# Kernel optimization log

Measured on AMD Instinct MI355X. Metric: run time of the kernel, lower is better.

## Reference

```python
import jax, jax.numpy as jnp
import numpy as np

C = 256
NUM_HEADS = 4
HEAD_DIM = C // NUM_HEADS
GROUPS = 32
EPS = 1e-5


def setup_inputs() -> dict:
    key = jax.random.key(0)
    ks = jax.random.split(key, 7)
    B, H, W = 4, 64, 64
    x = jax.random.normal(ks[0], (B, C, H, W), dtype=jnp.float32)
    gn_w = jax.random.normal(ks[1], (C,), dtype=jnp.float32) * 0.02 + 1.0
    gn_b = jax.random.normal(ks[2], (C,), dtype=jnp.float32) * 0.02
    qkv_w = jax.random.normal(ks[3], (3 * C, C), dtype=jnp.float32) * (1.0 / np.sqrt(C))
    qkv_b = jax.random.normal(ks[4], (3 * C,), dtype=jnp.float32) * 0.02
    out_w = jax.random.normal(ks[5], (C, C), dtype=jnp.float32) * (1.0 / np.sqrt(C))
    out_b = jax.random.normal(ks[6], (C,), dtype=jnp.float32) * 0.02
    return {"x": x, "gn_w": gn_w, "gn_b": gn_b, "qkv_w": qkv_w,
            "qkv_b": qkv_b, "out_w": out_w, "out_b": out_b}


def _group_norm(x, w, b):
    # x: [B, C, H, W]; normalize over (C/GROUPS, H, W) per group
    B, Cc, Hh, Ww = x.shape
    xg = x.reshape(B, GROUPS, Cc // GROUPS, Hh, Ww)
    mean = jnp.mean(xg, axis=(2, 3, 4), keepdims=True)
    var = jnp.var(xg, axis=(2, 3, 4), keepdims=True)
    xg = (xg - mean) * jax.lax.rsqrt(var + EPS)
    xn = xg.reshape(B, Cc, Hh, Ww)
    return xn * w[None, :, None, None] + b[None, :, None, None]


def reference(x, gn_w, gn_b, qkv_w, qkv_b, out_w, out_b):
    B, Cc, Hh, Ww = x.shape
    N = Hh * Ww
    h = _group_norm(x, gn_w, gn_b).reshape(B, Cc, N)
    # qkv conv1d (kernel size 1) == pointwise linear over channel dim
    qkv = jnp.einsum('oc,bcn->bon', qkv_w, h) + qkv_b[None, :, None]
    q, k, v = jnp.split(qkv, 3, axis=1)
    q = q.reshape(B, NUM_HEADS, HEAD_DIM, N)
    k = k.reshape(B, NUM_HEADS, HEAD_DIM, N)
    v = v.reshape(B, NUM_HEADS, HEAD_DIM, N)
    scale = 1.0 / np.sqrt(HEAD_DIM)
    attn = jnp.einsum('bhdk,bhdl->bhkl', q, k) * scale  # [B, H, N, N]
    attn = jax.nn.softmax(attn, axis=-1)
    out = jnp.einsum('bhkl,bhdl->bhdk', attn, v)  # [B, H, D, N]
    out = out.reshape(B, Cc, N)
    out = jnp.einsum('oc,bcn->bon', out_w, out) + out_b[None, :, None]
    return x + out.reshape(B, Cc, Hh, Ww)
```

## Files before the change

### kernel.cpp

```cpp
#include <hip/hip_runtime.h>
#include <cstdint>

typedef __bf16 bf16_t;
typedef __bf16 bf16x4 __attribute__((ext_vector_type(4)));
typedef __bf16 bf16x8 __attribute__((ext_vector_type(8)));
typedef float f32x4 __attribute__((ext_vector_type(4)));
typedef unsigned int u32x2 __attribute__((ext_vector_type(2)));
typedef unsigned int u32x4 __attribute__((ext_vector_type(4)));

#define B_ 4
#define C_ 256
#define N_ 4096
#define NH_ 4
#define HD_ 64

static __device__ __forceinline__ f32x4 mfma_bf16(bf16x8 a, bf16x8 b, f32x4 c) {
  return __builtin_amdgcn_mfma_f32_16x16x32_bf16(a, b, c, 0, 0, 0);
}

static __device__ __forceinline__ void async16(const void* g, void* l) {
  __builtin_amdgcn_global_load_lds(
      (__attribute__((address_space(1))) void*)(uintptr_t)g,
      (__attribute__((address_space(3))) void*)(uint32_t)(uintptr_t)l,
      16, 0, 0);
}

static __device__ __forceinline__ float fexp2(float x) {
#if __has_builtin(__builtin_amdgcn_exp2f)
  return __builtin_amdgcn_exp2f(x);
#else
  return exp2f(x);
#endif
}

static __device__ __forceinline__ unsigned pack_bf16(float lo, float hi) {
  bf16x4 t;
  t[0] = (bf16_t)lo;
  t[1] = (bf16_t)hi;
  return *(unsigned*)&t;
}

__global__ __launch_bounds__(256) void k_gn_stats(const float* __restrict__ x,
                                                  const float* __restrict__ gn_w,
                                                  const float* __restrict__ gn_b,
                                                  float* __restrict__ gnscale,
                                                  float* __restrict__ gnshift) {
  const int bg = blockIdx.x;
  const int b = bg >> 5, g = bg & 31;
  const float4* p4 = (const float4*)(x + (size_t)(b * C_ + g * 8) * N_);
  float s = 0.f, ss = 0.f;
  for (int i = threadIdx.x; i < 8192; i += 256) {
    float4 v = p4[i];
    s += (v.x + v.y) + (v.z + v.w);
    ss += (v.x * v.x + v.y * v.y) + (v.z * v.z + v.w * v.w);
  }
  for (int off = 32; off > 0; off >>= 1) {
    s += __shfl_down(s, off);
    ss += __shfl_down(ss, off);
  }
  __shared__ float red_s[4], red_ss[4];
  const int wid = threadIdx.x >> 6, lane = threadIdx.x & 63;
  if (lane == 0) { red_s[wid] = s; red_ss[wid] = ss; }
  __syncthreads();
  if (threadIdx.x < 8) {
    float S = (red_s[0] + red_s[1]) + (red_s[2] + red_s[3]);
    float SS = (red_ss[0] + red_ss[1]) + (red_ss[2] + red_ss[3]);
    float mean = S * (1.f / 32768.f);
    float var = SS * (1.f / 32768.f) - mean * mean;
    float rstd = rsqrtf(var + 1e-5f);
    int c = g * 8 + threadIdx.x;
    float w = gn_w[c];
    gnscale[b * C_ + c] = w * rstd;
    gnshift[b * C_ + c] = gn_b[c] - mean * rstd * w;
  }
}

__global__ __launch_bounds__(256) void k_conv_w(const float* __restrict__ qkv_w,
                                                const float* __restrict__ out_w,
                                                bf16_t* __restrict__ w1,
                                                bf16_t* __restrict__ w2) {
  int i = blockIdx.x * 256 + threadIdx.x;
  if (i < 3 * C_ * C_) w1[i] = (bf16_t)qkv_w[i];
  else w2[i - 3 * C_ * C_] = (bf16_t)out_w[i - 3 * C_ * C_];
}

__global__ __launch_bounds__(256) void k_gn_apply(const float* __restrict__ x,
                                                  const float* __restrict__ gnscale,
                                                  const float* __restrict__ gnshift,
                                                  bf16_t* __restrict__ h) {
  __shared__ bf16_t T[32 * 258];
  const int t = threadIdx.x;
  const int tok0 = blockIdx.x * 32;
  const int b = tok0 >> 12;
  const int n0 = tok0 & (N_ - 1);
  const int nl = t & 31, cset = t >> 5;
  const float* xb = x + ((size_t)(b * C_ + cset * 32) << 12) + n0 + nl;
  const float* scp = gnscale + b * C_ + cset * 32;
  const float* shp = gnshift + b * C_ + cset * 32;
#pragma unroll
  for (int j = 0; j < 32; ++j) {
    float y = xb[(size_t)j << 12] * scp[j] + shp[j];
    T[nl * 258 + cset * 32 + j] = (bf16_t)y;
  }
  __syncthreads();
  const int c4 = t & 63;
#pragma unroll
  for (int p = 0; p < 8; ++p) {
    const int tokl = p * 4 + (t >> 6);
    const int idx = tokl * 258 + c4 * 4;
    uint2 v;
    v.x = *(const unsigned*)&T[idx];
    v.y = *(const unsigned*)&T[idx + 2];
    *(uint2*)(h + ((size_t)(tok0 + tokl) << 8) + c4 * 4) = v;
  }
}

__global__ __launch_bounds__(256) void k_gemm_qkv(const bf16_t* __restrict__ h,
                                                  const bf16_t* __restrict__ w1,
                                                  const float* __restrict__ qkv_b,
                                                  bf16_t* __restrict__ Qb,
                                                  bf16_t* __restrict__ Kb,
                                                  bf16_t* __restrict__ Vb) {
  __shared__ bf16_t As[128 * 32], Bs[128 * 32];
  const int tid = threadIdx.x, lane = tid & 63, wid = tid >> 6;
  const int g = lane >> 4, q = lane & 15;
  const int wm = wid >> 1, wn = wid & 1;
  const int m0 = blockIdx.x * 128;
  const int o0 = blockIdx.y * 128;
  f32x4 acc[4][4] = {};
  const int srow = lane >> 2, scol = (lane & 3) * 8;
  for (int kc = 0; kc < 8; ++kc) {
    const int k0 = kc * 32;
#pragma unroll
    for (int j = 0; j < 2; ++j) {
      const int chunk = wid + j * 4;
      async16(h + (size_t)(m0 + chunk * 16 + srow) * C_ + k0 + scol, &As[chunk * 512]);
      async16(w1 + (size_t)(o0 + chunk * 16 + srow) * C_ + k0 + scol, &Bs[chunk * 512]);
    }
    __syncthreads();
    bf16x8 a[4], bb[4];
#pragma unroll
    for (int t = 0; t < 4; ++t) {
      a[t] = *(const bf16x8*)&As[(wm * 64 + t * 16 + q) * 32 + g * 8];
      bb[t] = *(const bf16x8*)&Bs[(wn * 64 + t * 16 + q) * 32 + g * 8];
    }
#pragma unroll
    for (int mi = 0; mi < 4; ++mi)
#pragma unroll
      for (int ni = 0; ni < 4; ++ni)
        acc[mi][ni] = mfma_bf16(a[mi], bb[ni], acc[mi][ni]);
    __syncthreads();
  }
  const float QSCALE = 0.1803368801111244f;
#pragma unroll
  for (int ni = 0; ni < 4; ++ni) {
    const int o = o0 + wn * 64 + ni * 16 + q;
    const float bias = qkv_b[o];
    const int mat = o >> 8;
    const int c = o & 255, hh = c >> 6, d = c & 63;
#pragma unroll
    for (int mi = 0; mi < 4; ++mi) {
      const int tokb = m0 + wm * 64 + mi * 16 + g * 4;
      const int b = tokb >> 12, n = tokb & (N_ - 1);
      const size_t bh = (size_t)(b * NH_ + hh);
      f32x4 t = acc[mi][ni] + bias;
      if (mat == 0) {
#pragma unroll
        for (int r = 0; r < 4; ++r)
          Qb[(bh * N_ + n + r) * HD_ + d] = (bf16_t)(t[r] * QSCALE);
      } else if (mat == 1) {
#pragma unroll
        for (int r = 0; r < 4; ++r)
          Kb[(bh * N_ + n + r) * HD_ + d] = (bf16_t)t[r];
      } else {
        *(bf16x4*)(Vb + (bh * HD_ + d) * N_ + n) = __builtin_convertvector(t, bf16x4);
      }
    }
  }
}

__global__ __launch_bounds__(512) void k_attn(const bf16_t* __restrict__ Qb,
                                              const bf16_t* __restrict__ Kb,
                                              const bf16_t* __restrict__ Vb,
                                              bf16_t* __restrict__ op0,
                                              bf16_t* __restrict__ op1,
                                              bf16_t* __restrict__ op23,
                                              float* __restrict__ lsum) {
  __shared__ __align__(16) bf16_t Ks[2][4096];
  __shared__ __align__(16) bf16_t Vs[2][4096];
  const int tid = threadIdx.x, lane = tid & 63, wid = tid >> 6;
  const int g = lane >> 4, q = lane & 15;
  const int qs = q & 7;
  int bid = blockIdx.x;
  bid = (bid & 7) * 128 + (bid >> 3);
  const int kh = bid & 3;
  const int qt = (bid >> 2) & 15;
  const int bh = bid >> 6;
  const int nq0 = qt * 256 + wid * 32;
  const int k00 = kh * (N_ / 4);
  const int NT = (N_ / 4) / 64;
  const size_t base = (size_t)bh << 18;
  const bf16_t* Qp = Qb + base;
  const bf16_t* Kp = Kb + base;
  const bf16_t* Vp = Vb + base;

  const bf16x8 bqA0 = *(const bf16x8*)(Qp + (size_t)(nq0 + q) * HD_ + g * 8);
  const bf16x8 bqA1 = *(const bf16x8*)(Qp + (size_t)(nq0 + q) * HD_ + 32 + g * 8);
  const bf16x8 bqB0 = *(const bf16x8*)(Qp + (size_t)(nq0 + 16 + q) * HD_ + g * 8);
  const bf16x8 bqB1 = *(const bf16x8*)(Qp + (size_t)(nq0 + 16 + q) * HD_ + 32 + g * 8);

  const int srow = lane >> 3;
  const int sc16 = (lane & 7) ^ srow;

  f32x4 laccA = {}, laccB = {};
  f32x4 accA[4] = {}, accB[4] = {};
  bf16x8 ones;
#pragma unroll
  for (int i = 0; i < 8; ++i) ones[i] = (bf16_t)1.0f;

  async16(Kp + (size_t)(k00 + wid * 8 + srow) * HD_ + sc16 * 8, &Ks[0][wid * 512]);
  async16(Vp + (size_t)(wid * 8 + srow) * N_ + k00 + sc16 * 8, &Vs[0][wid * 512]);
  __syncthreads();

  const bf16_t* kS = Kp + (size_t)(k00 + 64 + wid * 8 + srow) * HD_ + sc16 * 8;
  const bf16_t* vS = Vp + (size_t)(wid * 8 + srow) * N_ + k00 + 64 + sc16 * 8;

  for (int t = 0; t < NT; ++t) {
    const int buf = t & 1;
    if (t < NT - 1) {
      async16(kS, &Ks[buf ^ 1][wid * 512]);
      async16(vS, &Vs[buf ^ 1][wid * 512]);
      kS += 64 * HD_;
      vS += 64;
    }
    const bf16_t* Kl = Ks[buf];
    const bf16_t* Vl = Vs[buf];
    f32x4 z = {0.f, 0.f, 0.f, 0.f};
    f32x4 sA[4], sB[4];
    __builtin_amdgcn_s_setprio(1);
#pragma unroll
    for (int kb = 0; kb < 4; ++kb) {
      bf16x8 k0 = *(const bf16x8*)(Kl + (kb * 16 + q) * 64 + ((g ^ qs) * 8));
      bf16x8 k1 = *(const bf16x8*)(Kl + (kb * 16 + q) * 64 + (((4 + g) ^ qs) * 8));
      sA[kb] = mfma_bf16(k0, bqA0, z);
      sB[kb] = mfma_bf16(k0, bqB0, z);
      sA[kb] = mfma_bf16(k1, bqA1, sA[kb]);
      sB[kb] = mfma_bf16(k1, bqB1, sB[kb]);
    }
    __builtin_amdgcn_s_setprio(0);
#pragma unroll
    for (int kb = 0; kb < 4; ++kb)
#pragma unroll
      for (int r = 0; r < 4; ++r) {
        sA[kb][r] = fexp2(sA[kb][r]);
        sB[kb][r] = fexp2(sB[kb][r]);
      }
    bf16x8 pbA[2], pbB[2];
#pragma unroll
    for (int s = 0; s < 2; ++s) {
      const f32x4* st = s ? sB : sA;
      bf16x8* pb = s ? pbB : pbA;
#pragma unroll
      for (int h = 0; h < 2; ++h) {
        unsigned u0 = pack_bf16(st[2 * h][0], st[2 * h][1]);
        unsigned u1 = pack_bf16(st[2 * h][2], st[2 * h][3]);
        unsigned u2 = pack_bf16(st[2 * h + 1][0], st[2 * h + 1][1]);
        unsigned u3 = pack_bf16(st[2 * h + 1][2], st[2 * h + 1][3]);
        u32x4 w;
#if __has_builtin(__builtin_amdgcn_permlane32_swap) && __has_builtin(__builtin_amdgcn_permlane16_swap)
        u32x2 a02 = __builtin_amdgcn_permlane32_swap(u0, u2, false, false);
        u32x2 r02 = __builtin_amdgcn_permlane16_swap(a02[0], a02[1], false, false);
        u32x2 a13 = __builtin_amdgcn_permlane32_swap(u1, u3, false, false);
        u32x2 r13 = __builtin_amdgcn_permlane16_swap(a13[0], a13[1], false, false);
        w[0] = r02[0]; w[2] = r02[1]; w[1] = r13[0]; w[3] = r13[1];
#else
        const int sl0 = (g & 1) * 32 + q, sl1 = sl0 + 16;
        w[0] = (g < 2) ? __shfl((int)u0, sl0) : __shfl((int)u2, sl0);
        w[1] = (g < 2) ? __shfl((int)u1, sl0) : __shfl((int)u3, sl0);
        w[2] = (g < 2) ? __shfl((int)u0, sl1) : __shfl((int)u2, sl1);
        w[3] = (g < 2) ? __shfl((int)u1, sl1) : __shfl((int)u3, sl1);
#endif
        pb[h] = *(bf16x8*)&w;
      }
    }
    __builtin_amdgcn_s_setprio(1);
    laccA = mfma_bf16(ones, pbA[0], laccA);
    laccA = mfma_bf16(ones, pbA[1], laccA);
    laccB = mfma_bf16(ones, pbB[0], laccB);
    laccB = mfma_bf16(ones, pbB[1], laccB);
#pragma unroll
    for (int db = 0; db < 4; ++db) {
      bf16x8 v0 = *(const bf16x8*)(Vl + (db * 16 + q) * 64 + ((g ^ qs) * 8));
      bf16x8 v1 = *(const bf16x8*)(Vl + (db * 16 + q) * 64 + (((4 + g) ^ qs) * 8));
      accA[db] = mfma_bf16(v0, pbA[0], accA[db]);
      accB[db] = mfma_bf16(v0, pbB[0], accB[db]);
      accA[db] = mfma_bf16(v1, pbA[1], accA[db]);
      accB[db] = mfma_bf16(v1, pbB[1], accB[db]);
    }
    __builtin_amdgcn_s_setprio(0);
    __syncthreads();
  }

  bf16_t* Op;
  if (kh == 0) Op = op0 + (size_t)bh * N_ * HD_;
  else if (kh == 1) Op = op1 + (size_t)bh * N_ * HD_;
  else Op = op23 + (size_t)((kh - 2) * 16 + bh) * N_ * HD_;
  bf16_t* opA = Op + (size_t)(nq0 + q) * HD_;
  bf16_t* opB = opA + 16 * HD_;
#pragma unroll
  for (int db = 0; db < 4; ++db) {
    *(bf16x4*)(opA + db * 16 + g * 4) = __builtin_convertvector(accA[db], bf16x4);
    *(bf16x4*)(opB + db * 16 + g * 4) = __builtin_convertvector(accB[db], bf16x4);
  }
  if (g == 0) {
    const size_t mlb = (size_t)(kh * 16 + bh) * N_;
    lsum[mlb + nq0 + q] = laccA[0];
    lsum[mlb + nq0 + 16 + q] = laccB[0];
  }
}

__global__ __launch_bounds__(256) void k_attn_combine(const bf16_t* __restrict__ op0,
                                                      const bf16_t* __restrict__ op1,
                                                      const bf16_t* __restrict__ op23,
                                                      const float* __restrict__ lsum,
                                                      bf16_t* __restrict__ att) {
  const int gid = blockIdx.x * 256 + threadIdx.x;
  const int d8 = gid & 7;
  const int q = (gid >> 3) & (N_ - 1);
  const int bh = gid >> 15;
  const size_t ro = ((size_t)bh * N_ + q) * HD_ + d8 * 8;
  const float l = lsum[(size_t)bh * N_ + q] + lsum[(size_t)(16 + bh) * N_ + q] +
                  lsum[(size_t)(32 + bh) * N_ + q] + lsum[(size_t)(48 + bh) * N_ + q];
  const float inv = 1.0f / l;
  const bf16x8 o0 = *(const bf16x8*)(op0 + ro);
  const bf16x8 o1 = *(const bf16x8*)(op1 + ro);
  const bf16x8 o2 = *(const bf16x8*)(op23 + ro);
  const bf16x8 o3 = *(const bf16x8*)(op23 + (size_t)16 * N_ * HD_ + ro);
  bf16x8 r;
#pragma unroll
  for (int j = 0; j < 8; ++j)
    r[j] = (bf16_t)((((float)o0[j] + (float)o1[j]) + ((float)o2[j] + (float)o3[j])) * inv);
  const int b = bh >> 2, hh = bh & 3;
  *(bf16x8*)(att + ((size_t)b * N_ + q) * C_ + hh * HD_ + d8 * 8) = r;
}

__global__ __launch_bounds__(256) void k_gemm_out(const bf16_t* __restrict__ att,
                                                  const bf16_t* __restrict__ w2,
                                                  const float* __restrict__ out_b,
                                                  const float* __restrict__ x,
                                                  float* __restrict__ out) {
  __shared__ bf16_t As[128 * 32], Bs[128 * 32];
  const int tid = threadIdx.x, lane = tid & 63, wid = tid >> 6;
  const int g = lane >> 4, q = lane & 15;
  const int wm = wid >> 1, wn = wid & 1;
  const int m0 = blockIdx.x * 128;
  const int o0 = blockIdx.y * 128;
  f32x4 acc[4][4] = {};
  const int srow = lane >> 2, scol = (lane & 3) * 8;
  for (int kc = 0; kc < 8; ++kc) {
    const int k0 = kc * 32;
#pragma unroll
    for (int j = 0; j < 2; ++j) {
      const int chunk = wid + j * 4;
      async16(att + (size_t)(m0 + chunk * 16 + srow) * C_ + k0 + scol, &As[chunk * 512]);
      async16(w2 + (size_t)(o0 + chunk * 16 + srow) * C_ + k0 + scol, &Bs[chunk * 512]);
    }
    __syncthreads();
    bf16x8 a[4], bb[4];
#pragma unroll
    for (int t = 0; t < 4; ++t) {
      a[t] = *(const bf16x8*)&As[(wm * 64 + t * 16 + q) * 32 + g * 8];
      bb[t] = *(const bf16x8*)&Bs[(wn * 64 + t * 16 + q) * 32 + g * 8];
    }
#pragma unroll
    for (int mi = 0; mi < 4; ++mi)
#pragma unroll
      for (int ni = 0; ni < 4; ++ni)
        acc[mi][ni] = mfma_bf16(a[mi], bb[ni], acc[mi][ni]);
    __syncthreads();
  }
#pragma unroll
  for (int ni = 0; ni < 4; ++ni) {
    const int o = o0 + wn * 64 + ni * 16 + q;
    const float bias = out_b[o];
#pragma unroll
    for (int mi = 0; mi < 4; ++mi) {
      const int tokb = m0 + wm * 64 + mi * 16 + g * 4;
      const int b = tokb >> 12, n = tokb & (N_ - 1);
      const size_t idx = ((size_t)(b * C_ + o) << 12) + n;
      const float4 xv = *(const float4*)(x + idx);
      f32x4 t = acc[mi][ni];
      float4 r = make_float4(t[0] + bias + xv.x, t[1] + bias + xv.y,
                             t[2] + bias + xv.z, t[3] + bias + xv.w);
      *(float4*)(out + idx) = r;
    }
  }
}

extern "C" void kernel_launch(void* const* d_in, const int* in_sizes, int n_in,
                              void* d_out, int out_size, void* d_ws, size_t ws_size,
                              hipStream_t stream) {
  (void)in_sizes; (void)n_in; (void)out_size; (void)ws_size;
  const float* x = (const float*)d_in[0];
  const float* gn_w = (const float*)d_in[1];
  const float* gn_b = (const float*)d_in[2];
  const float* qkv_w = (const float*)d_in[3];
  const float* qkv_b = (const float*)d_in[4];
  const float* out_w = (const float*)d_in[5];
  const float* out_b = (const float*)d_in[6];
  float* out = (float*)d_out;

  char* ws = (char*)d_ws;
  float* gnscale = (float*)ws;
  float* gnshift = gnscale + 1024;
  bf16_t* w1bf = (bf16_t*)(ws + 8192);
  bf16_t* w2bf = w1bf + 196608;
  bf16_t* hbuf = w2bf + 65536;
  bf16_t* Qb = hbuf + 4194304;
  bf16_t* Kb = Qb + 4194304;
  bf16_t* Vb = Kb + 4194304;
  bf16_t* op1 = Vb + 4194304;
  float* lsum = (float*)(op1 + 4194304);
  bf16_t* op23 = (bf16_t*)d_out;

  k_gn_stats<<<128, 256, 0, stream>>>(x, gn_w, gn_b, gnscale, gnshift);
  k_conv_w<<<1024, 256, 0, stream>>>(qkv_w, out_w, w1bf, w2bf);
  k_gn_apply<<<512, 256, 0, stream>>>(x, gnscale, gnshift, hbuf);
  k_gemm_qkv<<<dim3(128, 6), 256, 0, stream>>>(hbuf, w1bf, qkv_b, Qb, Kb, Vb);
  k_attn<<<1024, 512, 0, stream>>>(Qb, Kb, Vb, hbuf, op1, op23, lsum);
  k_attn_combine<<<2048, 256, 0, stream>>>(hbuf, op1, op23, lsum, Qb);
  k_gemm_out<<<dim3(128, 2), 256, 0, stream>>>(Qb, w2bf, out_b, x, out);
}
```

Baseline: 127.4 us.

## Load K/V tiles directly from global memory instead of LDS double-buffering

Removes the LDS staging of K and V tiles (async global-to-LDS copies with double buffering and a barrier every iteration). Each wave now reads its K and V fragments straight from global memory through the cache. Blocks shrink from 512 to 256 threads and the grid doubles to match. The barriers and LDS footprint go away, but every wave now issues its own redundant global/L2 loads of the same K/V data with exposed latency and no cross-wave sharing.

```diff
diff --git a/kernel.cpp b/kernel.cpp
--- a/kernel.cpp
+++ b/kernel.cpp
@@ -179,24 +179,21 @@
   }
 }
 
-__global__ __launch_bounds__(512) void k_attn(const bf16_t* __restrict__ Qb,
+__global__ __launch_bounds__(256) void k_attn(const bf16_t* __restrict__ Qb,
                                               const bf16_t* __restrict__ Kb,
                                               const bf16_t* __restrict__ Vb,
                                               bf16_t* __restrict__ op0,
                                               bf16_t* __restrict__ op1,
                                               bf16_t* __restrict__ op23,
                                               float* __restrict__ lsum) {
-  __shared__ __align__(16) bf16_t Ks[2][4096];
-  __shared__ __align__(16) bf16_t Vs[2][4096];
   const int tid = threadIdx.x, lane = tid & 63, wid = tid >> 6;
   const int g = lane >> 4, q = lane & 15;
-  const int qs = q & 7;
   int bid = blockIdx.x;
-  bid = (bid & 7) * 128 + (bid >> 3);
+  bid = (bid & 7) * 256 + (bid >> 3);
   const int kh = bid & 3;
-  const int qt = (bid >> 2) & 15;
-  const int bh = bid >> 6;
-  const int nq0 = qt * 256 + wid * 32;
+  const int qt = (bid >> 2) & 31;
+  const int bh = bid >> 7;
+  const int nq0 = qt * 128 + wid * 32;
   const int k00 = kh * (N_ / 4);
   const int NT = (N_ / 4) / 64;
   const size_t base = (size_t)bh << 18;
@@ -209,45 +206,31 @@
   const bf16x8 bqB0 = *(const bf16x8*)(Qp + (size_t)(nq0 + 16 + q) * HD_ + g * 8);
   const bf16x8 bqB1 = *(const bf16x8*)(Qp + (size_t)(nq0 + 16 + q) * HD_ + 32 + g * 8);
 
-  const int srow = lane >> 3;
-  const int sc16 = (lane & 7) ^ srow;
-
   f32x4 laccA = {}, laccB = {};
   f32x4 accA[4] = {}, accB[4] = {};
   bf16x8 ones;
 #pragma unroll
   for (int i = 0; i < 8; ++i) ones[i] = (bf16_t)1.0f;
 
-  async16(Kp + (size_t)(k00 + wid * 8 + srow) * HD_ + sc16 * 8, &Ks[0][wid * 512]);
-  async16(Vp + (size_t)(wid * 8 + srow) * N_ + k00 + sc16 * 8, &Vs[0][wid * 512]);
-  __syncthreads();
-
-  const bf16_t* kS = Kp + (size_t)(k00 + 64 + wid * 8 + srow) * HD_ + sc16 * 8;
-  const bf16_t* vS = Vp + (size_t)(wid * 8 + srow) * N_ + k00 + 64 + sc16 * 8;
+  const bf16_t* kRow = Kp + (size_t)(k00 + q) * HD_;
+  const bf16_t* vRow = Vp + (size_t)q * N_ + k00;
 
   for (int t = 0; t < NT; ++t) {
-    const int buf = t & 1;
-    if (t < NT - 1) {
-      async16(kS, &Ks[buf ^ 1][wid * 512]);
-      async16(vS, &Vs[buf ^ 1][wid * 512]);
-      kS += 64 * HD_;
-      vS += 64;
-    }
-    const bf16_t* Kl = Ks[buf];
-    const bf16_t* Vl = Vs[buf];
+    const int nk0 = t * 64;
     f32x4 z = {0.f, 0.f, 0.f, 0.f};
     f32x4 sA[4], sB[4];
-    __builtin_amdgcn_s_setprio(1);
 #pragma unroll
     for (int kb = 0; kb < 4; ++kb) {
-      bf16x8 k0 = *(const bf16x8*)(Kl + (kb * 16 + q) * 64 + ((g ^ qs) * 8));
-      bf16x8 k1 = *(const bf16x8*)(Kl + (kb * 16 + q) * 64 + (((4 + g) ^ qs) * 8));
+      const bf16_t* kr = kRow + (size_t)(nk0 + kb * 16) * HD_;
+      bf16x8 k0 = *(const bf16x8*)(kr + g * 8);
+      bf16x8 k1 = *(const bf16x8*)(kr + 32 + g * 8);
+      __builtin_amdgcn_s_setprio(1);
       sA[kb] = mfma_bf16(k0, bqA0, z);
       sB[kb] = mfma_bf16(k0, bqB0, z);
       sA[kb] = mfma_bf16(k1, bqA1, sA[kb]);
       sB[kb] = mfma_bf16(k1, bqB1, sB[kb]);
-    }
-    __builtin_amdgcn_s_setprio(0);
+      __builtin_amdgcn_s_setprio(0);
+    }
 #pragma unroll
     for (int kb = 0; kb < 4; ++kb)
 #pragma unroll
@@ -288,17 +271,19 @@
     laccA = mfma_bf16(ones, pbA[1], laccA);
     laccB = mfma_bf16(ones, pbB[0], laccB);
     laccB = mfma_bf16(ones, pbB[1], laccB);
+    __builtin_amdgcn_s_setprio(0);
 #pragma unroll
     for (int db = 0; db < 4; ++db) {
-      bf16x8 v0 = *(const bf16x8*)(Vl + (db * 16 + q) * 64 + ((g ^ qs) * 8));
-      bf16x8 v1 = *(const bf16x8*)(Vl + (db * 16 + q) * 64 + (((4 + g) ^ qs) * 8));
+      const bf16_t* vr = vRow + (size_t)(db * 16) * N_ + nk0;
+      bf16x8 v0 = *(const bf16x8*)(vr + g * 8);
+      bf16x8 v1 = *(const bf16x8*)(vr + 32 + g * 8);
+      __builtin_amdgcn_s_setprio(1);
       accA[db] = mfma_bf16(v0, pbA[0], accA[db]);
       accB[db] = mfma_bf16(v0, pbB[0], accB[db]);
       accA[db] = mfma_bf16(v1, pbA[1], accA[db]);
       accB[db] = mfma_bf16(v1, pbB[1], accB[db]);
-    }
-    __builtin_amdgcn_s_setprio(0);
-    __syncthreads();
+      __builtin_amdgcn_s_setprio(0);
+    }
   }
 
   bf16_t* Op;
@@ -427,7 +412,7 @@
   k_conv_w<<<1024, 256, 0, stream>>>(qkv_w, out_w, w1bf, w2bf);
   k_gn_apply<<<512, 256, 0, stream>>>(x, gnscale, gnshift, hbuf);
   k_gemm_qkv<<<dim3(128, 6), 256, 0, stream>>>(hbuf, w1bf, qkv_b, Qb, Kb, Vb);
-  k_attn<<<1024, 512, 0, stream>>>(Qb, Kb, Vb, hbuf, op1, op23, lsum);
+  k_attn<<<2048, 256, 0, stream>>>(Qb, Kb, Vb, hbuf, op1, op23, lsum);
   k_attn_combine<<<2048, 256, 0, stream>>>(hbuf, op1, op23, lsum, Qb);
   k_gemm_out<<<dim3(128, 2), 256, 0, stream>>>(Qb, w2bf, out_b, x, out);
 }
```

After: 306.6 us. +140.6%, slower.

## Halve attention key split, merge GN-stats with weight conversion, drop setprio

Applied to the files above, without the earlier changes.

The attention kernel now splits the key range into 2 chunks instead of 4, so it runs 512 blocks that each loop over twice as many key tiles. The combine step then reads two partials instead of four. The GroupNorm statistics kernel and the weight-to-bf16 conversion kernel are merged into one launch, and the s_setprio hints around the MFMA sections are removed. This cuts partial-output traffic, combine work and one launch, but with fewer blocks on the GPU it risks lower occupancy and load balance in the attention kernel.

```diff
diff --git a/kernel.cpp b/kernel.cpp
--- a/kernel.cpp
+++ b/kernel.cpp
@@ -40,11 +40,22 @@
   return *(unsigned*)&t;
 }
 
-__global__ __launch_bounds__(256) void k_gn_stats(const float* __restrict__ x,
-                                                  const float* __restrict__ gn_w,
-                                                  const float* __restrict__ gn_b,
-                                                  float* __restrict__ gnscale,
-                                                  float* __restrict__ gnshift) {
+__global__ __launch_bounds__(256) void k_pre(const float* __restrict__ x,
+                                             const float* __restrict__ gn_w,
+                                             const float* __restrict__ gn_b,
+                                             const float* __restrict__ qkv_w,
+                                             const float* __restrict__ out_w,
+                                             float* __restrict__ gnscale,
+                                             float* __restrict__ gnshift,
+                                             bf16_t* __restrict__ w1,
+                                             bf16_t* __restrict__ w2) {
+  __shared__ float red_s[4], red_ss[4];
+  if (blockIdx.x >= 128) {
+    int i = (blockIdx.x - 128) * 256 + threadIdx.x;
+    if (i < 3 * C_ * C_) w1[i] = (bf16_t)qkv_w[i];
+    else w2[i - 3 * C_ * C_] = (bf16_t)out_w[i - 3 * C_ * C_];
+    return;
+  }
   const int bg = blockIdx.x;
   const int b = bg >> 5, g = bg & 31;
   const float4* p4 = (const float4*)(x + (size_t)(b * C_ + g * 8) * N_);
@@ -58,7 +69,6 @@
     s += __shfl_down(s, off);
     ss += __shfl_down(ss, off);
   }
-  __shared__ float red_s[4], red_ss[4];
   const int wid = threadIdx.x >> 6, lane = threadIdx.x & 63;
   if (lane == 0) { red_s[wid] = s; red_ss[wid] = ss; }
   __syncthreads();
@@ -73,15 +83,6 @@
     gnscale[b * C_ + c] = w * rstd;
     gnshift[b * C_ + c] = gn_b[c] - mean * rstd * w;
   }
-}
-
-__global__ __launch_bounds__(256) void k_conv_w(const float* __restrict__ qkv_w,
-                                                const float* __restrict__ out_w,
-                                                bf16_t* __restrict__ w1,
-                                                bf16_t* __restrict__ w2) {
-  int i = blockIdx.x * 256 + threadIdx.x;
-  if (i < 3 * C_ * C_) w1[i] = (bf16_t)qkv_w[i];
-  else w2[i - 3 * C_ * C_] = (bf16_t)out_w[i - 3 * C_ * C_];
 }
 
 __global__ __launch_bounds__(256) void k_gn_apply(const float* __restrict__ x,
@@ -184,7 +185,6 @@
                                               const bf16_t* __restrict__ Vb,
                                               bf16_t* __restrict__ op0,
                                               bf16_t* __restrict__ op1,
-                                              bf16_t* __restrict__ op23,
                                               float* __restrict__ lsum) {
   __shared__ __align__(16) bf16_t Ks[2][4096];
   __shared__ __align__(16) bf16_t Vs[2][4096];
@@ -192,13 +192,13 @@
   const int g = lane >> 4, q = lane & 15;
   const int qs = q & 7;
   int bid = blockIdx.x;
-  bid = (bid & 7) * 128 + (bid >> 3);
-  const int kh = bid & 3;
-  const int qt = (bid >> 2) & 15;
-  const int bh = bid >> 6;
+  bid = (bid & 7) * 64 + (bid >> 3);
+  const int kh = bid & 1;
+  const int qt = (bid >> 1) & 15;
+  const int bh = bid >> 5;
   const int nq0 = qt * 256 + wid * 32;
-  const int k00 = kh * (N_ / 4);
-  const int NT = (N_ / 4) / 64;
+  const int k00 = kh * (N_ / 2);
+  const int NT = (N_ / 2) / 64;
   const size_t base = (size_t)bh << 18;
   const bf16_t* Qp = Qb + base;
   const bf16_t* Kp = Kb + base;
@@ -237,7 +237,6 @@
     const bf16_t* Vl = Vs[buf];
     f32x4 z = {0.f, 0.f, 0.f, 0.f};
     f32x4 sA[4], sB[4];
-    __builtin_amdgcn_s_setprio(1);
 #pragma unroll
     for (int kb = 0; kb < 4; ++kb) {
       bf16x8 k0 = *(const bf16x8*)(Kl + (kb * 16 + q) * 64 + ((g ^ qs) * 8));
@@ -247,7 +246,6 @@
       sA[kb] = mfma_bf16(k1, bqA1, sA[kb]);
       sB[kb] = mfma_bf16(k1, bqB1, sB[kb]);
     }
-    __builtin_amdgcn_s_setprio(0);
 #pragma unroll
     for (int kb = 0; kb < 4; ++kb)
 #pragma unroll
@@ -283,7 +281,6 @@
         pb[h] = *(bf16x8*)&w;
       }
     }
-    __builtin_amdgcn_s_setprio(1);
     laccA = mfma_bf16(ones, pbA[0], laccA);
     laccA = mfma_bf16(ones, pbA[1], laccA);
     laccB = mfma_bf16(ones, pbB[0], laccB);
@@ -297,14 +294,10 @@
       accA[db] = mfma_bf16(v1, pbA[1], accA[db]);
       accB[db] = mfma_bf16(v1, pbB[1], accB[db]);
     }
-    __builtin_amdgcn_s_setprio(0);
     __syncthreads();
   }
 
-  bf16_t* Op;
-  if (kh == 0) Op = op0 + (size_t)bh * N_ * HD_;
-  else if (kh == 1) Op = op1 + (size_t)bh * N_ * HD_;
-  else Op = op23 + (size_t)((kh - 2) * 16 + bh) * N_ * HD_;
+  bf16_t* Op = (kh == 0 ? op0 : op1) + (size_t)bh * N_ * HD_;
   bf16_t* opA = Op + (size_t)(nq0 + q) * HD_;
   bf16_t* opB = opA + 16 * HD_;
 #pragma unroll
@@ -321,7 +314,6 @@
 
 __global__ __launch_bounds__(256) void k_attn_combine(const bf16_t* __restrict__ op0,
                                                       const bf16_t* __restrict__ op1,
-                                                      const bf16_t* __restrict__ op23,
                                                       const float* __restrict__ lsum,
                                                       bf16_t* __restrict__ att) {
   const int gid = blockIdx.x * 256 + threadIdx.x;
@@ -329,17 +321,14 @@
   const int q = (gid >> 3) & (N_ - 1);
   const int bh = gid >> 15;
   const size_t ro = ((size_t)bh * N_ + q) * HD_ + d8 * 8;
-  const float l = lsum[(size_t)bh * N_ + q] + lsum[(size_t)(16 + bh) * N_ + q] +
-                  lsum[(size_t)(32 + bh) * N_ + q] + lsum[(size_t)(48 + bh) * N_ + q];
+  const float l = lsum[(size_t)bh * N_ + q] + lsum[(size_t)(16 + bh) * N_ + q];
   const float inv = 1.0f / l;
   const bf16x8 o0 = *(const bf16x8*)(op0 + ro);
   const bf16x8 o1 = *(const bf16x8*)(op1 + ro);
-  const bf16x8 o2 = *(const bf16x8*)(op23 + ro);
-  const bf16x8 o3 = *(const bf16x8*)(op23 + (size_t)16 * N_ * HD_ + ro);
   bf16x8 r;
 #pragma unroll
   for (int j = 0; j < 8; ++j)
-    r[j] = (bf16_t)((((float)o0[j] + (float)o1[j]) + ((float)o2[j] + (float)o3[j])) * inv);
+    r[j] = (bf16_t)(((float)o0[j] + (float)o1[j]) * inv);
   const int b = bh >> 2, hh = bh & 3;
   *(bf16x8*)(att + ((size_t)b * N_ + q) * C_ + hh * HD_ + d8 * 8) = r;
 }
@@ -421,13 +410,11 @@
   bf16_t* Vb = Kb + 4194304;
   bf16_t* op1 = Vb + 4194304;
   float* lsum = (float*)(op1 + 4194304);
-  bf16_t* op23 = (bf16_t*)d_out;
-
-  k_gn_stats<<<128, 256, 0, stream>>>(x, gn_w, gn_b, gnscale, gnshift);
-  k_conv_w<<<1024, 256, 0, stream>>>(qkv_w, out_w, w1bf, w2bf);
+
+  k_pre<<<1152, 256, 0, stream>>>(x, gn_w, gn_b, qkv_w, out_w, gnscale, gnshift, w1bf, w2bf);
   k_gn_apply<<<512, 256, 0, stream>>>(x, gnscale, gnshift, hbuf);
   k_gemm_qkv<<<dim3(128, 6), 256, 0, stream>>>(hbuf, w1bf, qkv_b, Qb, Kb, Vb);
-  k_attn<<<1024, 512, 0, stream>>>(Qb, Kb, Vb, hbuf, op1, op23, lsum);
-  k_attn_combine<<<2048, 256, 0, stream>>>(hbuf, op1, op23, lsum, Qb);
+  k_attn<<<512, 512, 0, stream>>>(Qb, Kb, Vb, hbuf, op1, lsum);
+  k_attn_combine<<<2048, 256, 0, stream>>>(hbuf, op1, lsum, Qb);
   k_gemm_out<<<dim3(128, 2), 256, 0, stream>>>(Qb, w2bf, out_b, x, out);
 }
```

After: 121.7 us. 4.4% less time.
